# Kernel tuning notes

Hardware: AMD Instinct MI355X
Metric: run time of the kernel (lower is better)

## Reference

```python
import jax, jax.numpy as jnp
import numpy as np
from jax import lax

TOTAL_STEPS = 100
BETA_0 = 0.1
BETA_1 = 20.0


def setup_inputs() -> dict:
    key = jax.random.key(0)
    k1, k2 = jax.random.split(key)
    x = jax.random.normal(k1, (64, 256, 64), dtype=jnp.float32)
    noise = jax.random.normal(k2, (TOTAL_STEPS, 64, 256, 64), dtype=jnp.float32)
    return {"x": x, "noise": noise}


def reference(x, noise):
    # VP-SDE Euler-Maruyama forward diffusion, matching forward_sample.
    S = TOTAL_STEPS
    dt = jnp.float32(1.0 / S)
    sqrt_dt = jnp.sqrt(dt)
    # torch loop uses t in [1..S] and computes coefficients at (t-1)/S
    norm_t = (jnp.arange(S, dtype=jnp.float32)) / S  # (t-1)/S for t=1..S

    def step(x_prev, inp):
        nt, n = inp
        beta_t = BETA_0 + nt * (BETA_1 - BETA_0)
        drift = -0.5 * beta_t * x_prev
        x_t = x_prev + drift * dt + jnp.sqrt(beta_t) * n * sqrt_dt
        return x_t, x_t

    _, traj = lax.scan(step, x, (norm_t, noise))  # traj: (S, N, L, D)
    return jnp.concatenate([x[None], traj], axis=0)  # (S+1, N, L, D)
```

## Files before the change

### kernel.cpp

```cpp
#include <hip/hip_runtime.h>
#include <math.h>
#include <stdint.h>


#define S_STEPS 100
#define U 4
#define NWIN (S_STEPS / U)

typedef float f32x4 __attribute__((ext_vector_type(4)));

#define WAITV(n) asm volatile("s_waitcnt vmcnt(" #n ")" ::: "memory")

__device__ __forceinline__ void gl_lds16(const float* g, const float* l) {
    __builtin_amdgcn_global_load_lds(
        (const __attribute__((address_space(1))) unsigned int*)g,
        (__attribute__((address_space(3))) unsigned int*)l,
        16, 0, 0);
}

__global__ __launch_bounds__(256) void vpsde_fwd_kernel(
    const float* __restrict__ x,
    const float* __restrict__ noise,
    float* __restrict__ out,
    int ne)
{
    __shared__ __align__(16) float s_noise[2][U][4][256];
    __shared__ float2 s_ab[S_STEPS];

    const int tid  = threadIdx.x;
    const int wid  = tid >> 6;
    const int lane = tid & 63;

    if (tid < S_STEPS) {
        const float dt = 0.01f;
        float nt_  = (float)tid * dt;
        float beta = 0.1f + nt_ * 19.9f;
        s_ab[tid] = make_float2(1.0f - 0.5f * beta * dt,
                                sqrtf(beta) * 0.1f);
    }
    __syncthreads();

    const size_t idx4  = (size_t)blockIdx.x * 256 + tid;
    const size_t plane = (size_t)ne;

    f32x4 xv = *(const f32x4*)(x + idx4 * 4);
    __builtin_nontemporal_store(xv, (f32x4*)(out + idx4 * 4));

    const float* gld = noise + idx4 * 4;
    float*       dst = out + plane + idx4 * 4;

    auto issue = [&](int b) {
        #pragma unroll
        for (int k = 0; k < U; ++k) {
            gl_lds16(gld, &s_noise[b][k][wid][0]);
            gld += plane;
        }
    };
    auto consume = [&](int b, int t0) {
        #pragma unroll
        for (int k = 0; k < U; ++k) {
            float2 ab = s_ab[t0 + k];
            f32x4 nv = *(const f32x4*)&s_noise[b][k][wid][lane * 4];
            xv = ab.x * xv + ab.y * nv;
            __builtin_nontemporal_store(xv, (f32x4*)dst);
            dst += plane;
        }
    };

    issue(0);
    issue(1);

    WAITV(4);
    __builtin_amdgcn_sched_barrier(0);
    consume(0, 0);
    __builtin_amdgcn_sched_barrier(0);
    issue(0);

    int b = 1;
    for (int w = 1; w <= NWIN - 2; ++w) {
        WAITV(8);
        __builtin_amdgcn_sched_barrier(0);
        consume(b, w * U);
        __builtin_amdgcn_sched_barrier(0);
        if (w <= NWIN - 3) issue(b);
        b ^= 1;
    }

    WAITV(4);
    __builtin_amdgcn_sched_barrier(0);
    consume(b, (NWIN - 1) * U);
}

extern "C" void kernel_launch(void* const* d_in, const int* in_sizes, int n_in,
                              void* d_out, int out_size, void* d_ws, size_t ws_size,
                              hipStream_t stream) {
    const float* x     = (const float*)d_in[0];
    const float* noise = (const float*)d_in[1];
    float* out         = (float*)d_out;

    const int ne  = in_sizes[0];
    const int ne4 = ne / 4;
    const int block = 256;
    const int grid  = ne4 / block;

    vpsde_fwd_kernel<<<grid, block, 0, stream>>>(x, noise, out, ne);
}
```

Baseline: 192.1 us.

## Warp-specialize into producer waves loading noise and consumer waves computing

Splits each block into two producer waves that stream noise tiles into double-buffered LDS via global_load_lds and two consumer waves that run the recurrence and store outputs, synchronized with block barriers per window. Each block now covers 128 float4 columns instead of 256, so the grid doubles. The aim is to decouple load latency from compute and store issue. In exchange, half the waves do no arithmetic, and every window adds a block-wide barrier.

```diff
diff --git a/kernel.cpp b/kernel.cpp
--- a/kernel.cpp
+++ b/kernel.cpp
@@ -1,6 +1,5 @@
 #include <hip/hip_runtime.h>
 #include <math.h>
-#include <stdint.h>
 
 
 #define S_STEPS 100
@@ -9,9 +8,7 @@
 
 typedef float f32x4 __attribute__((ext_vector_type(4)));
 
-#define WAITV(n) asm volatile("s_waitcnt vmcnt(" #n ")" ::: "memory")
-
-__device__ __forceinline__ void gl_lds16(const float* g, const float* l) {
+__device__ __forceinline__ void gl_lds16(const float* g, float* l) {
     __builtin_amdgcn_global_load_lds(
         (const __attribute__((address_space(1))) unsigned int*)g,
         (__attribute__((address_space(3))) unsigned int*)l,
@@ -24,7 +21,7 @@
     float* __restrict__ out,
     int ne)
 {
-    __shared__ __align__(16) float s_noise[2][U][4][256];
+    __shared__ __align__(16) float s_noise[2][U][512];
     __shared__ float2 s_ab[S_STEPS];
 
     const int tid  = threadIdx.x;
@@ -40,55 +37,58 @@
     }
     __syncthreads();
 
-    const size_t idx4  = (size_t)blockIdx.x * 256 + tid;
     const size_t plane = (size_t)ne;
+    const int    ne4   = ne >> 2;
 
-    f32x4 xv = *(const f32x4*)(x + idx4 * 4);
-    __builtin_nontemporal_store(xv, (f32x4*)(out + idx4 * 4));
+    if (wid < 2) {
+        const float* gsrc = noise + (size_t)blockIdx.x * 512 + wid * 256
+                          + lane * 4;
 
-    const float* gld = noise + idx4 * 4;
-    float*       dst = out + plane + idx4 * 4;
+        #pragma unroll
+        for (int k = 0; k < U; ++k)
+            gl_lds16(gsrc + (size_t)k * plane, &s_noise[0][k][wid * 256]);
+        gsrc += (size_t)U * plane;
+        asm volatile("s_waitcnt vmcnt(0)" ::: "memory");
 
-    auto issue = [&](int b) {
-        #pragma unroll
-        for (int k = 0; k < U; ++k) {
-            gl_lds16(gld, &s_noise[b][k][wid][0]);
-            gld += plane;
+        for (int w = 0; w < NWIN; ++w) {
+            __builtin_amdgcn_s_barrier();
+            if (w + 1 < NWIN) {
+                #pragma unroll
+                for (int k = 0; k < U; ++k)
+                    gl_lds16(gsrc + (size_t)k * plane,
+                             &s_noise[(w + 1) & 1][k][wid * 256]);
+                gsrc += (size_t)U * plane;
+            }
+            asm volatile("s_waitcnt vmcnt(0)" ::: "memory");
         }
-    };
-    auto consume = [&](int b, int t0) {
-        #pragma unroll
-        for (int k = 0; k < U; ++k) {
-            float2 ab = s_ab[t0 + k];
-            f32x4 nv = *(const f32x4*)&s_noise[b][k][wid][lane * 4];
-            xv = ab.x * xv + ab.y * nv;
-            __builtin_nontemporal_store(xv, (f32x4*)dst);
-            dst += plane;
+    } else {
+        const int    c  = (wid - 2) * 64 + lane;
+        const size_t g4 = (size_t)blockIdx.x * 128 + c;
+        const f32x4* x4   = (const f32x4*)x;
+        f32x4*       out4 = (f32x4*)out;
+
+        f32x4 xv = x4[g4];
+        __builtin_nontemporal_store(xv, out4 + g4);
+
+        f32x4* dst = out4 + (size_t)ne4 + g4;
+        int t = 0;
+        for (int w = 0; w < NWIN; ++w) {
+            __builtin_amdgcn_s_barrier();
+            f32x4 nv[U];
+            #pragma unroll
+            for (int k = 0; k < U; ++k)
+                nv[k] = *(const f32x4*)&s_noise[w & 1][k][c * 4];
+            #pragma unroll
+            for (int k = 0; k < U; ++k) {
+                float2 ab = s_ab[t + k];
+                xv = ab.x * xv + ab.y * nv[k];
+                __builtin_nontemporal_store(xv, dst);
+                dst += ne4;
+            }
+            t += U;
+            asm volatile("s_waitcnt lgkmcnt(0)" ::: "memory");
         }
-    };
-
-    issue(0);
-    issue(1);
-
-    WAITV(4);
-    __builtin_amdgcn_sched_barrier(0);
-    consume(0, 0);
-    __builtin_amdgcn_sched_barrier(0);
-    issue(0);
-
-    int b = 1;
-    for (int w = 1; w <= NWIN - 2; ++w) {
-        WAITV(8);
-        __builtin_amdgcn_sched_barrier(0);
-        consume(b, w * U);
-        __builtin_amdgcn_sched_barrier(0);
-        if (w <= NWIN - 3) issue(b);
-        b ^= 1;
     }
-
-    WAITV(4);
-    __builtin_amdgcn_sched_barrier(0);
-    consume(b, (NWIN - 1) * U);
 }
 
 extern "C" void kernel_launch(void* const* d_in, const int* in_sizes, int n_in,
@@ -101,7 +101,7 @@
     const int ne  = in_sizes[0];
     const int ne4 = ne / 4;
     const int block = 256;
-    const int grid  = ne4 / block;
+    const int grid  = ne4 / 128;
 
     vpsde_fwd_kernel<<<grid, block, 0, stream>>>(x, noise, out, ne);
 }
```

After: 189.7 us. No clear change (-1.2%).
